# Optimization experiments

Hardware: AMD Instinct MI355X
Metric: run time of the kernel (lower is better)

The kernel has to match this reference:

```python
import jax, jax.numpy as jnp
import numpy as np

D_MODEL = 2048
N_HEADS = 16
D_HEAD = 128
BATCH = 2
SEQ = 2048
INIT_STD = 0.02
N_LAYERS = 12


def setup_inputs() -> dict:
    key = jax.random.key(0)
    ks = jax.random.split(key, 5)
    attn_std = INIT_STD
    proj_std = INIT_STD / np.sqrt(2 * N_LAYERS)
    return {
        "normalized_resid_pre": jax.random.normal(ks[0], (BATCH, SEQ, D_MODEL), jnp.float32),
        "W_Q": jax.random.normal(ks[1], (N_HEADS, D_MODEL, D_HEAD), jnp.float32) * attn_std,
        "W_K": jax.random.normal(ks[2], (N_HEADS, D_MODEL, D_HEAD), jnp.float32) * attn_std,
        "W_V": jax.random.normal(ks[3], (N_HEADS, D_MODEL, D_HEAD), jnp.float32) * attn_std,
        "W_O": jax.random.normal(ks[4], (N_HEADS, D_HEAD, D_MODEL), jnp.float32) * proj_std,
        "b_Q": jnp.zeros((N_HEADS, D_HEAD), jnp.float32),
        "b_K": jnp.zeros((N_HEADS, D_HEAD), jnp.float32),
        "b_V": jnp.zeros((N_HEADS, D_HEAD), jnp.float32),
        "b_O": jnp.zeros((D_MODEL,), jnp.float32),
    }


def reference(normalized_resid_pre, W_Q, W_K, W_V, W_O, b_Q, b_K, b_V, b_O):
    x = normalized_resid_pre
    # q,k,v: [batch, posn, nheads, d_head]
    q = jnp.einsum('bsd,hde->bshe', x, W_Q) + b_Q
    k = jnp.einsum('bsd,hde->bshe', x, W_K) + b_K
    v = jnp.einsum('bsd,hde->bshe', x, W_V) + b_V
    # scores: [batch, nheads, posn_Q, posn_K]
    scores = jnp.einsum('bqhe,bkhe->bhqk', q, k) / jnp.sqrt(jnp.float32(D_HEAD))
    S = scores.shape[-1]
    causal = jnp.tril(jnp.ones((S, S), bool))
    scores = jnp.where(causal, scores, jnp.float32(-jnp.inf))
    pattern = jax.nn.softmax(scores, axis=-1)
    z = jnp.einsum('bhqk,bkhe->bqhe', pattern, v)
    attn_out = jnp.einsum('bqhe,hed->bqd', z, W_O) + b_O
    return attn_out
```

## Files before the change

kernel.cpp:

```cpp
#include <hip/hip_runtime.h>
#include <hip/hip_bf16.h>

typedef __hip_bfloat16 bf16;
typedef __attribute__((ext_vector_type(8))) short bf16x8;
typedef __attribute__((ext_vector_type(4))) short bf16x4;
typedef __attribute__((ext_vector_type(4))) float f32x4;

#define D_MODEL 2048
#define SEQ     2048
#define NH      16
#define DH      128
#define BATCH   2
#define MTOT    (BATCH*SEQ)

__device__ __forceinline__ void async_cp16(const bf16* g, bf16* l) {
    __builtin_amdgcn_global_load_lds(
        (const __attribute__((address_space(1))) void*)g,
        (__attribute__((address_space(3))) void*)l, 16, 0, 0);
}

__device__ __forceinline__ short bf16bits(float f) {
    bf16 b = __float2bfloat16(f);
    return *reinterpret_cast<short*>(&b);
}

__global__ __launch_bounds__(256) void cvt_k(const float* __restrict__ in,
                                             bf16* __restrict__ out) {
    const long i = ((long)blockIdx.x * 256 + threadIdx.x) * 8;
    float4 a = *(const float4*)(in + i);
    float4 b = *(const float4*)(in + i + 4);
    __align__(16) bf16 t[8];
    t[0] = __float2bfloat16(a.x); t[1] = __float2bfloat16(a.y);
    t[2] = __float2bfloat16(a.z); t[3] = __float2bfloat16(a.w);
    t[4] = __float2bfloat16(b.x); t[5] = __float2bfloat16(b.y);
    t[6] = __float2bfloat16(b.z); t[7] = __float2bfloat16(b.w);
    *(bf16x8*)(out + i) = *(const bf16x8*)t;
}

__global__ __launch_bounds__(256) void transpose_cvt3_k(
    const float* __restrict__ in0, const float* __restrict__ in1,
    const float* __restrict__ in2,
    bf16* __restrict__ out, int R, int Cn, int mats_per_src)
{
    __shared__ float t[32][33];
    const int z = blockIdx.z;
    const int src = z / mats_per_src, mat = z % mats_per_src;
    const float* in = (src == 0) ? in0 : (src == 1) ? in1 : in2;
    const float* inm = in + (long)mat * R * Cn;
    bf16* outm = out + (long)z * R * Cn;
    const int c0 = blockIdx.x * 32, r0 = blockIdx.y * 32;
    const int tx = threadIdx.x & 31, ty = threadIdx.x >> 5;
#pragma unroll
    for (int i = 0; i < 4; ++i)
        t[ty + i*8][tx] = inm[(long)(r0 + ty + i*8) * Cn + c0 + tx];
    __syncthreads();
#pragma unroll
    for (int i = 0; i < 4; ++i)
        outm[(long)(c0 + ty + i*8) * R + r0 + tx] = __float2bfloat16(t[tx][ty + i*8]);
}

__global__ __launch_bounds__(256) void transpose_v_k(
    const bf16* __restrict__ V, bf16* __restrict__ VT)
{
    __shared__ bf16 t[32][33];
    const int bh = blockIdx.z;
    const int b = bh >> 4, h = bh & 15;
    const bf16* inm = V + (long)b*SEQ*D_MODEL + h*DH;
    bf16* outm = VT + (long)bh*DH*SEQ;
    const int r0 = blockIdx.x * 32;
    const int c0 = blockIdx.y * 32;
    const int tx = threadIdx.x & 31, ty = threadIdx.x >> 5;
#pragma unroll
    for (int i = 0; i < 4; ++i)
        t[ty + i*8][tx] = inm[(long)(r0 + ty + i*8)*D_MODEL + c0 + tx];
    __syncthreads();
#pragma unroll
    for (int i = 0; i < 4; ++i)
        outm[(long)(c0 + ty + i*8)*SEQ + r0 + tx] = t[tx][ty + i*8];
}

template <bool C_F32>
__device__ __forceinline__ void gemm128x128(
    const bf16* __restrict__ A, int lda,
    const bf16* __restrict__ Bt, int ldb,
    void* __restrict__ C, int ldc,
    const float* __restrict__ bias,
    int Kdim, int m0, int n0)
{
    __shared__ __align__(16) bf16 As[128*32];
    __shared__ __align__(16) bf16 Bs[128*32];
    const int tid  = threadIdx.x;
    const int wave = tid >> 6, lane = tid & 63;
    const int lr = lane & 15, lq = lane >> 4;
    const int wrow = wave >> 1, wcol = wave & 1;
    const int sr = lane >> 2, sk = (lane & 3) * 8;

    const f32x4 zero4 = {0.f, 0.f, 0.f, 0.f};
    f32x4 acc[4][4];
#pragma unroll
    for (int i = 0; i < 4; ++i)
#pragma unroll
        for (int j = 0; j < 4; ++j) acc[i][j] = zero4;

    for (int k0 = 0; k0 < Kdim; k0 += 32) {
#pragma unroll
        for (int c = 0; c < 2; ++c) {
            const int r = wave*32 + c*16;
            async_cp16(A  + (long)(m0 + r + sr)*lda + k0 + sk, As + r*32);
            async_cp16(Bt + (long)(n0 + r + sr)*ldb + k0 + sk, Bs + r*32);
        }
        __syncthreads();
        bf16x8 af[4], bfr[4];
#pragma unroll
        for (int i = 0; i < 4; ++i)
            af[i] = *(const bf16x8*)(As + (wrow*64 + i*16 + lr)*32 + lq*8);
#pragma unroll
        for (int j = 0; j < 4; ++j)
            bfr[j] = *(const bf16x8*)(Bs + (wcol*64 + j*16 + lr)*32 + lq*8);
#pragma unroll
        for (int i = 0; i < 4; ++i)
#pragma unroll
            for (int j = 0; j < 4; ++j)
                acc[i][j] = __builtin_amdgcn_mfma_f32_16x16x32_bf16(af[i], bfr[j], acc[i][j], 0, 0, 0);
        __syncthreads();
    }
#pragma unroll
    for (int j = 0; j < 4; ++j) {
        const int col = n0 + wcol*64 + j*16 + lr;
        const float bv = bias[col];
#pragma unroll
        for (int i = 0; i < 4; ++i) {
            const int row = m0 + wrow*64 + i*16 + lq*4;
#pragma unroll
            for (int r = 0; r < 4; ++r) {
                const float v = acc[i][j][r] + bv;
                if constexpr (C_F32) ((float*)C)[(long)(row + r)*ldc + col] = v;
                else ((bf16*)C)[(long)(row + r)*ldc + col] = __float2bfloat16(v);
            }
        }
    }
}

__global__ __launch_bounds__(256) void qkv_gemm_k(
    const bf16* __restrict__ X, const bf16* __restrict__ WT3,
    const float* __restrict__ bQ, const float* __restrict__ bK, const float* __restrict__ bV,
    bf16* __restrict__ Qo, bf16* __restrict__ Ko, bf16* __restrict__ Vo)
{
    const int mt  = blockIdx.x;
    const int sel = blockIdx.y >> 4;
    const int h   = blockIdx.y & 15;
    const float* bias; bf16* C;
    if (sel == 0)      { bias = bQ; C = Qo; }
    else if (sel == 1) { bias = bK; C = Ko; }
    else               { bias = bV; C = Vo; }
    gemm128x128<false>(X, D_MODEL, WT3 + (long)blockIdx.y*DH*D_MODEL, D_MODEL,
                       C + h*DH, NH*DH, bias + h*DH, D_MODEL, mt*128, 0);
}

__global__ __launch_bounds__(256) void out_gemm_k(
    const bf16* __restrict__ Z, const bf16* __restrict__ WOT,
    const float* __restrict__ bO, float* __restrict__ Out)
{
    gemm128x128<true>(Z, D_MODEL, WOT, D_MODEL, Out, D_MODEL, bO, D_MODEL,
                      (int)blockIdx.x*128, (int)blockIdx.y*128);
}

__global__ __launch_bounds__(512) void flash_k(
    const bf16* __restrict__ Q, const bf16* __restrict__ K,
    const bf16* __restrict__ VT, bf16* __restrict__ Z)
{
    __shared__ __align__(16) bf16 Ks[64*128];
    __shared__ __align__(16) bf16 Vts[128*64];
    __shared__ __align__(16) bf16 Ps[128*72];

    const int qt = (int)(gridDim.x - 1) - (int)blockIdx.x;
    const int bh = blockIdx.y;
    const int b  = bh >> 4, h = bh & 15;
    const long base = (long)b*SEQ*D_MODEL + h*DH;
    const bf16* Qb  = Q + base;
    const bf16* Kb  = K + base;
    const bf16* VTb = VT + (long)bh*DH*SEQ;
    bf16* Zb = Z + base;
    const int q0 = qt*128;
    const int tid = threadIdx.x, wave = tid >> 6, lane = tid & 63;
    const int lr = lane & 15, lq = lane >> 4;
    const int rx = lr & 7;

    const int ks_key_off = lane >> 4;
    const int ks_slot    = lane & 15;
    const int vt_row_off = lane >> 3;
    const int vt_slot    = lane & 7;

    bf16x8 aq[4];
#pragma unroll
    for (int ks = 0; ks < 4; ++ks)
        aq[ks] = *(const bf16x8*)(Qb + (long)(q0 + wave*16 + lr)*D_MODEL + ks*32 + lq*8);

    const f32x4 zero4 = {0.f, 0.f, 0.f, 0.f};
    f32x4 o_acc[8];
#pragma unroll
    for (int jf = 0; jf < 8; ++jf) o_acc[jf] = zero4;
    float m_run = -1e30f, l_run = 0.f;

    const float scale = 0.08838834764831845f;
    const int NT = 2*qt + 2;

    for (int kt = 0; kt < NT; ++kt) {
        const int k0 = kt*64;
        __syncthreads();
#pragma unroll
        for (int c2 = 0; c2 < 2; ++c2) {
            const int c = wave*2 + c2;
            const int key = c*4 + ks_key_off;
            async_cp16(Kb + (long)(k0 + key)*D_MODEL + ((ks_slot ^ (key & 7)) * 8),
                       Ks + c*512);
            const int f = c*8 + vt_row_off;
            async_cp16(VTb + (long)f*SEQ + k0 + ((vt_slot ^ (f & 7)) * 8),
                       Vts + c*512);
        }
        __syncthreads();

        const int rel_hi = q0 + wave*16 + 15 - k0;
        if (rel_hi >= 0) {
            f32x4 sc[4];
#pragma unroll
            for (int mt = 0; mt < 4; ++mt) sc[mt] = zero4;
            __builtin_amdgcn_s_setprio(1);
#pragma unroll
            for (int mt = 0; mt < 4; ++mt)
#pragma unroll
                for (int ks = 0; ks < 4; ++ks) {
                    bf16x8 bk = *(const bf16x8*)(Ks + (mt*16 + lr)*128 + (((ks*4 + lq) ^ rx) * 8));
                    sc[mt] = __builtin_amdgcn_mfma_f32_16x16x32_bf16(bk, aq[ks], sc[mt], 0, 0, 0);
                }
            __builtin_amdgcn_s_setprio(0);

            if (rel_hi < 78) {
                const int rel = q0 + wave*16 + lr - k0;
#pragma unroll
                for (int mt = 0; mt < 4; ++mt)
#pragma unroll
                    for (int r = 0; r < 4; ++r)
                        if (mt*16 + lq*4 + r > rel) sc[mt][r] = -1e30f;
            }

            float mx = sc[0][0];
#pragma unroll
            for (int mt = 0; mt < 4; ++mt)
#pragma unroll
                for (int r = 0; r < 4; ++r) mx = fmaxf(mx, sc[mt][r]);
            mx = fmaxf(mx, __shfl_xor(mx, 16, 64));
            mx = fmaxf(mx, __shfl_xor(mx, 32, 64));
            mx *= scale;

            if (!__all(mx - m_run <= 8.0f)) {
                const float mn = fmaxf(m_run, mx);
                const float al = __expf(m_run - mn);
                l_run *= al;
#pragma unroll
                for (int jf = 0; jf < 8; ++jf)
#pragma unroll
                    for (int r = 0; r < 4; ++r) o_acc[jf][r] *= al;
                m_run = mn;
            }

            float rs = 0.f;
#pragma unroll
            for (int mt = 0; mt < 4; ++mt)
#pragma unroll
                for (int r = 0; r < 4; ++r) {
                    const float p = __expf(fmaf(sc[mt][r], scale, -m_run));
                    sc[mt][r] = p;
                    rs += p;
                }
            rs += __shfl_xor(rs, 16, 64);
            rs += __shfl_xor(rs, 32, 64);
            l_run += rs;

#pragma unroll
            for (int mt = 0; mt < 4; ++mt) {
                bf16x4 pk;
#pragma unroll
                for (int r = 0; r < 4; ++r) pk[r] = bf16bits(sc[mt][r]);
                *(bf16x4*)(Ps + (wave*16 + lr)*72 + mt*16 + lq*4) = pk;
            }

            bf16x8 pb0 = *(const bf16x8*)(Ps + (wave*16 + lr)*72 + lq*8);
            bf16x8 pb1 = *(const bf16x8*)(Ps + (wave*16 + lr)*72 + 32 + lq*8);

            __builtin_amdgcn_s_setprio(1);
#pragma unroll
            for (int jf = 0; jf < 8; ++jf) {
                const int f = jf*16 + lr;
                bf16x8 av0 = *(const bf16x8*)(Vts + f*64 + ((lq ^ rx) * 8));
                bf16x8 av1 = *(const bf16x8*)(Vts + f*64 + (((4 + lq) ^ rx) * 8));
                o_acc[jf] = __builtin_amdgcn_mfma_f32_16x16x32_bf16(av0, pb0, o_acc[jf], 0, 0, 0);
                o_acc[jf] = __builtin_amdgcn_mfma_f32_16x16x32_bf16(av1, pb1, o_acc[jf], 0, 0, 0);
            }
            __builtin_amdgcn_s_setprio(0);
        }
    }

    const float inv = 1.f / l_run;
    const long zrow = (long)(q0 + wave*16 + lr) * D_MODEL;
#pragma unroll
    for (int jf = 0; jf < 8; ++jf) {
        bf16x4 pk;
#pragma unroll
        for (int r = 0; r < 4; ++r) pk[r] = bf16bits(o_acc[jf][r] * inv);
        *(bf16x4*)(Zb + zrow + jf*16 + lq*4) = pk;
    }
}

extern "C" void kernel_launch(void* const* d_in, const int* in_sizes, int n_in,
                              void* d_out, int out_size, void* d_ws, size_t ws_size,
                              hipStream_t stream) {
    const float* X  = (const float*)d_in[0];
    const float* WQ = (const float*)d_in[1];
    const float* WK = (const float*)d_in[2];
    const float* WV = (const float*)d_in[3];
    const float* WO = (const float*)d_in[4];
    const float* bQ = (const float*)d_in[5];
    const float* bK = (const float*)d_in[6];
    const float* bV = (const float*)d_in[7];
    const float* bO = (const float*)d_in[8];
    float* out = (float*)d_out;

    bf16* ws = (bf16*)d_ws;
    const long WSZ = (long)NH*DH*D_MODEL;
    const long MSZ = (long)MTOT*D_MODEL;
    bf16* Xb  = ws;
    bf16* WT3 = Xb + MSZ;
    bf16* WOT = WT3 + 3*WSZ;
    bf16* Qb  = WOT + WSZ;
    bf16* Kb  = Qb + MSZ;
    bf16* Vb  = Kb + MSZ;
    bf16* Zb  = Xb;
    bf16* VT  = WT3;

    cvt_k<<<MSZ/(256*8), 256, 0, stream>>>(X, Xb);
    transpose_cvt3_k<<<dim3(DH/32, D_MODEL/32, 3*NH), 256, 0, stream>>>(
        WQ, WK, WV, WT3, D_MODEL, DH, NH);
    transpose_cvt3_k<<<dim3(D_MODEL/32, D_MODEL/32, 1), 256, 0, stream>>>(
        WO, WO, WO, WOT, D_MODEL, D_MODEL, 1);

    qkv_gemm_k<<<dim3(MTOT/128, 48), 256, 0, stream>>>(Xb, WT3, bQ, bK, bV, Qb, Kb, Vb);
    transpose_v_k<<<dim3(SEQ/32, DH/32, BATCH*NH), 256, 0, stream>>>(Vb, VT);
    flash_k<<<dim3(SEQ/128, BATCH*NH), 512, 0, stream>>>(Qb, Kb, VT, Zb);
    out_gemm_k<<<dim3(MTOT/128, D_MODEL/128), 256, 0, stream>>>(Zb, WOT, bO, out);
}
```

Before: 407.9 us.

## Replace QKV projection with 256x256-tile, 8-wave pipelined GEMM kernel

Swaps the 128x128 QKV GEMM for a new 256x256 tile kernel with 512 threads. It uses double-buffered async global-to-LDS loads with XOR swizzling, interleaves staging of the next K-slice with MFMA phases, and raises wave priority around the MFMA blocks. The larger tile raises arithmetic intensity and cuts redundant global reads of X and weights. In exchange it uses 128KB of LDS and 128 accumulator registers per thread, which limits occupancy, and the grid shrinks to 16x24 blocks.

```diff
diff --git a/kernel.cpp b/kernel.cpp
--- a/kernel.cpp
+++ b/kernel.cpp
@@ -23,6 +23,9 @@
     bf16 b = __float2bfloat16(f);
     return *reinterpret_cast<short*>(&b);
 }
+
+#define GBAR() do { asm volatile("" ::: "memory"); __builtin_amdgcn_s_barrier(); \
+                    asm volatile("" ::: "memory"); } while (0)
 
 __global__ __launch_bounds__(256) void cvt_k(const float* __restrict__ in,
                                              bf16* __restrict__ out) {
@@ -141,28 +144,157 @@
     }
 }
 
-__global__ __launch_bounds__(256) void qkv_gemm_k(
-    const bf16* __restrict__ X, const bf16* __restrict__ WT3,
-    const float* __restrict__ bQ, const float* __restrict__ bK, const float* __restrict__ bV,
-    bf16* __restrict__ Qo, bf16* __restrict__ Ko, bf16* __restrict__ Vo)
-{
-    const int mt  = blockIdx.x;
-    const int sel = blockIdx.y >> 4;
-    const int h   = blockIdx.y & 15;
-    const float* bias; bf16* C;
-    if (sel == 0)      { bias = bQ; C = Qo; }
-    else if (sel == 1) { bias = bK; C = Ko; }
-    else               { bias = bV; C = Vo; }
-    gemm128x128<false>(X, D_MODEL, WT3 + (long)blockIdx.y*DH*D_MODEL, D_MODEL,
-                       C + h*DH, NH*DH, bias + h*DH, D_MODEL, mt*128, 0);
-}
-
 __global__ __launch_bounds__(256) void out_gemm_k(
     const bf16* __restrict__ Z, const bf16* __restrict__ WOT,
     const float* __restrict__ bO, float* __restrict__ Out)
 {
     gemm128x128<true>(Z, D_MODEL, WOT, D_MODEL, Out, D_MODEL, bO, D_MODEL,
                       (int)blockIdx.x*128, (int)blockIdx.y*128);
+}
+
+__global__ __launch_bounds__(512, 2) void qkv_gemm256_k(
+    const bf16* __restrict__ A, const bf16* __restrict__ Bt,
+    const float* __restrict__ bQ, const float* __restrict__ bK, const float* __restrict__ bV,
+    bf16* __restrict__ Qo, bf16* __restrict__ Ko, bf16* __restrict__ Vo)
+{
+    __shared__ __align__(16) bf16 lds[65536];
+    bf16* As = lds;
+    bf16* Bs = lds + 32768;
+
+    const int m0 = blockIdx.x * 256;
+    const int n0 = blockIdx.y * 256;
+    const int tid = threadIdx.x, wave = tid >> 6, lane = tid & 63;
+    const int wm = wave >> 2, wn = wave & 3;
+    const int lr = lane & 15, lq = lane >> 4;
+    const int sph = (lr >> 1) & 3;
+
+    const int s_r  = lane >> 2;
+    const int s_sl = lane & 3;
+
+    auto stageA = [&](int t, int kh) {
+        const int k = t*64 + kh*32;
+        bf16* u = As + (((t & 1)*2 + kh) << 13);
+#pragma unroll
+        for (int i = 0; i < 2; ++i) {
+            const int c = wave*2 + i;
+            const int r = c*16 + s_r;
+            async_cp16(A + (long)(m0 + r)*D_MODEL + k + ((s_sl ^ ((r >> 1) & 3)) * 8),
+                       u + c*512);
+        }
+    };
+    auto stageB = [&](int t, int kh) {
+        const int k = t*64 + kh*32;
+        bf16* u = Bs + (((t & 1)*2 + kh) << 13);
+#pragma unroll
+        for (int i = 0; i < 2; ++i) {
+            const int c = wave*2 + i;
+            const int r = c*16 + s_r;
+            async_cp16(Bt + (long)(n0 + r)*D_MODEL + k + ((s_sl ^ ((r >> 1) & 3)) * 8),
+                       u + c*512);
+        }
+    };
+    auto rdA = [&](int t, int kh, int fm) -> bf16x8 {
+        const int r = wm*128 + fm*16 + lr;
+        return *(const bf16x8*)(As + (((t & 1)*2 + kh) << 13) + r*32 + ((lq ^ sph) * 8));
+    };
+    auto rdB = [&](int t, int kh, int fn) -> bf16x8 {
+        const int r = wn*64 + fn*16 + lr;
+        return *(const bf16x8*)(Bs + (((t & 1)*2 + kh) << 13) + r*32 + ((lq ^ sph) * 8));
+    };
+
+    const f32x4 zero4 = {0.f, 0.f, 0.f, 0.f};
+    f32x4 acc[8][4];
+#pragma unroll
+    for (int i = 0; i < 8; ++i)
+#pragma unroll
+        for (int j = 0; j < 4; ++j) acc[i][j] = zero4;
+
+    const int NT = D_MODEL / 64;
+
+    stageA(0, 0); stageB(0, 0);
+    stageA(0, 1); stageB(0, 1);
+    stageA(1, 0); stageB(1, 0);
+    asm volatile("s_waitcnt vmcnt(4)" ::: "memory");
+    GBAR();
+
+    for (int t = 0; t < NT; ++t) {
+        bf16x8 aF[4], bF[4];
+
+#pragma unroll
+        for (int j = 0; j < 4; ++j) aF[j] = rdA(t, 0, j);
+#pragma unroll
+        for (int j = 0; j < 4; ++j) bF[j] = rdB(t, 0, j);
+        if (t + 1 < NT) stageA(t + 1, 1);
+        GBAR();
+        __builtin_amdgcn_s_setprio(1);
+#pragma unroll
+        for (int j = 0; j < 4; ++j)
+#pragma unroll
+            for (int fn = 0; fn < 4; ++fn)
+                acc[j][fn] = __builtin_amdgcn_mfma_f32_16x16x32_bf16(aF[j], bF[fn], acc[j][fn], 0, 0, 0);
+        __builtin_amdgcn_s_setprio(0);
+        GBAR();
+
+#pragma unroll
+        for (int j = 0; j < 4; ++j) aF[j] = rdA(t, 0, 4 + j);
+        if (t + 1 < NT) stageB(t + 1, 1);
+        GBAR();
+        __builtin_amdgcn_s_setprio(1);
+#pragma unroll
+        for (int j = 0; j < 4; ++j)
+#pragma unroll
+            for (int fn = 0; fn < 4; ++fn)
+                acc[4 + j][fn] = __builtin_amdgcn_mfma_f32_16x16x32_bf16(aF[j], bF[fn], acc[4 + j][fn], 0, 0, 0);
+        __builtin_amdgcn_s_setprio(0);
+        GBAR();
+
+#pragma unroll
+        for (int j = 0; j < 4; ++j) aF[j] = rdA(t, 1, j);
+#pragma unroll
+        for (int j = 0; j < 4; ++j) bF[j] = rdB(t, 1, j);
+        if (t + 2 < NT) stageA(t + 2, 0);
+        GBAR();
+        __builtin_amdgcn_s_setprio(1);
+#pragma unroll
+        for (int j = 0; j < 4; ++j)
+#pragma unroll
+            for (int fn = 0; fn < 4; ++fn)
+                acc[j][fn] = __builtin_amdgcn_mfma_f32_16x16x32_bf16(aF[j], bF[fn], acc[j][fn], 0, 0, 0);
+        __builtin_amdgcn_s_setprio(0);
+        GBAR();
+
+#pragma unroll
+        for (int j = 0; j < 4; ++j) aF[j] = rdA(t, 1, 4 + j);
+        if (t + 2 < NT) stageB(t + 2, 0);
+        GBAR();
+        __builtin_amdgcn_s_setprio(1);
+#pragma unroll
+        for (int j = 0; j < 4; ++j)
+#pragma unroll
+            for (int fn = 0; fn < 4; ++fn)
+                acc[4 + j][fn] = __builtin_amdgcn_mfma_f32_16x16x32_bf16(aF[j], bF[fn], acc[4 + j][fn], 0, 0, 0);
+        __builtin_amdgcn_s_setprio(0);
+        if (t < NT - 2) asm volatile("s_waitcnt vmcnt(4)" ::: "memory");
+        else            asm volatile("s_waitcnt vmcnt(0)" ::: "memory");
+        GBAR();
+    }
+
+    const int gc0 = n0 + wn*64;
+    const int sel = gc0 >> 11;
+    bf16* C        = (sel == 0) ? Qo : (sel == 1) ? Ko : Vo;
+    const float* bs = (sel == 0) ? bQ : (sel == 1) ? bK : bV;
+#pragma unroll
+    for (int fn = 0; fn < 4; ++fn) {
+        const int dcol = (gc0 + fn*16 + lr) & 2047;
+        const float bv = bs[dcol];
+#pragma unroll
+        for (int fm = 0; fm < 8; ++fm) {
+            const int row = m0 + wm*128 + fm*16 + lq*4;
+#pragma unroll
+            for (int rr = 0; rr < 4; ++rr)
+                C[(long)(row + rr)*D_MODEL + dcol] = __float2bfloat16(acc[fm][fn][rr] + bv);
+        }
+    }
 }
 
 __global__ __launch_bounds__(512) void flash_k(
@@ -344,7 +476,8 @@
     transpose_cvt3_k<<<dim3(D_MODEL/32, D_MODEL/32, 1), 256, 0, stream>>>(
         WO, WO, WO, WOT, D_MODEL, D_MODEL, 1);
 
-    qkv_gemm_k<<<dim3(MTOT/128, 48), 256, 0, stream>>>(Xb, WT3, bQ, bK, bV, Qb, Kb, Vb);
+    qkv_gemm256_k<<<dim3(MTOT/256, 3*D_MODEL/256), 512, 0, stream>>>(
+        Xb, WT3, bQ, bK, bV, Qb, Kb, Vb);
     transpose_v_k<<<dim3(SEQ/32, DH/32, BATCH*NH), 256, 0, stream>>>(Vb, VT);
     flash_k<<<dim3(SEQ/128, BATCH*NH), 512, 0, stream>>>(Qb, Kb, VT, Zb);
     out_gemm_k<<<dim3(MTOT/128, D_MODEL/128), 256, 0, stream>>>(Zb, WOT, bO, out);
```

Result: no change. 410.6 us (+0.7%).

## Replace QKV GEMM with 128x256 tile, 8-wave, triple-buffered async-LDS kernel

Applied to the files above, without the earlier changes.

Replaces the 128x128-tile QKV projection kernel with a new kernel using 128x256 tiles, 512 threads, and a three-slot async global-to-LDS pipeline with an XOR-swizzled layout. A 1D grid is remapped so that blocks on the same XCD share N columns, which aims to improve L2 reuse. Fewer redundant A-tile loads and deeper prefetch are meant to raise MFMA utilization. In exchange the kernel needs more LDS and registers per block, which can lower occupancy.

```diff
diff --git a/kernel.cpp b/kernel.cpp
--- a/kernel.cpp
+++ b/kernel.cpp
@@ -23,6 +23,9 @@
     bf16 b = __float2bfloat16(f);
     return *reinterpret_cast<short*>(&b);
 }
+
+#define GBAR() do { asm volatile("" ::: "memory"); __builtin_amdgcn_s_barrier(); \
+                    asm volatile("" ::: "memory"); } while (0)
 
 __global__ __launch_bounds__(256) void cvt_k(const float* __restrict__ in,
                                              bf16* __restrict__ out) {
@@ -141,28 +144,116 @@
     }
 }
 
-__global__ __launch_bounds__(256) void qkv_gemm_k(
-    const bf16* __restrict__ X, const bf16* __restrict__ WT3,
-    const float* __restrict__ bQ, const float* __restrict__ bK, const float* __restrict__ bV,
-    bf16* __restrict__ Qo, bf16* __restrict__ Ko, bf16* __restrict__ Vo)
-{
-    const int mt  = blockIdx.x;
-    const int sel = blockIdx.y >> 4;
-    const int h   = blockIdx.y & 15;
-    const float* bias; bf16* C;
-    if (sel == 0)      { bias = bQ; C = Qo; }
-    else if (sel == 1) { bias = bK; C = Ko; }
-    else               { bias = bV; C = Vo; }
-    gemm128x128<false>(X, D_MODEL, WT3 + (long)blockIdx.y*DH*D_MODEL, D_MODEL,
-                       C + h*DH, NH*DH, bias + h*DH, D_MODEL, mt*128, 0);
-}
-
 __global__ __launch_bounds__(256) void out_gemm_k(
     const bf16* __restrict__ Z, const bf16* __restrict__ WOT,
     const float* __restrict__ bO, float* __restrict__ Out)
 {
     gemm128x128<true>(Z, D_MODEL, WOT, D_MODEL, Out, D_MODEL, bO, D_MODEL,
                       (int)blockIdx.x*128, (int)blockIdx.y*128);
+}
+
+__global__ __launch_bounds__(512) void qkv_gemm_k2(
+    const bf16* __restrict__ A, const bf16* __restrict__ Bt,
+    const float* __restrict__ bQ, const float* __restrict__ bK, const float* __restrict__ bV,
+    bf16* __restrict__ Qo, bf16* __restrict__ Ko, bf16* __restrict__ Vo)
+{
+    __shared__ __align__(16) bf16 lds[36864];
+    bf16* As = lds;
+    bf16* Bs = lds + 12288;
+
+    const int lin = blockIdx.x;
+    const int xcd = lin & 7, idx = lin >> 3;
+    const int m0 = (idx & 31) * 128;
+    const int n0 = (xcd * 3 + (idx >> 5)) * 256;
+
+    const int tid = threadIdx.x, wave = tid >> 6, lane = tid & 63;
+    const int wm = wave >> 2, wn = wave & 3;
+    const int lr = lane & 15, lq = lane >> 4;
+    const int sph = (lr >> 1) & 3;
+
+    const int s_r  = lane >> 2;
+    const int s_sl = lane & 3;
+
+    auto stageA = [&](int t, int slot) {
+        const int k = t * 32;
+        const int r = wave*16 + s_r;
+        async_cp16(A + (long)(m0 + r)*D_MODEL + k + ((s_sl ^ ((r >> 1) & 3)) * 8),
+                   As + slot*4096 + wave*512);
+    };
+    auto stageB = [&](int t, int slot) {
+        const int k = t * 32;
+#pragma unroll
+        for (int i = 0; i < 2; ++i) {
+            const int c = wave*2 + i;
+            const int r = c*16 + s_r;
+            async_cp16(Bt + (long)(n0 + r)*D_MODEL + k + ((s_sl ^ ((r >> 1) & 3)) * 8),
+                       Bs + slot*8192 + c*512);
+        }
+    };
+    auto rdA = [&](int slot, int fm) -> bf16x8 {
+        const int r = wm*64 + fm*16 + lr;
+        return *(const bf16x8*)(As + slot*4096 + r*32 + ((lq ^ sph) * 8));
+    };
+    auto rdB = [&](int slot, int fn) -> bf16x8 {
+        const int r = wn*64 + fn*16 + lr;
+        return *(const bf16x8*)(Bs + slot*8192 + r*32 + ((lq ^ sph) * 8));
+    };
+
+    const f32x4 zero4 = {0.f, 0.f, 0.f, 0.f};
+    f32x4 acc[4][4];
+#pragma unroll
+    for (int i = 0; i < 4; ++i)
+#pragma unroll
+        for (int j = 0; j < 4; ++j) acc[i][j] = zero4;
+
+    const int NT = D_MODEL / 32;
+
+    stageA(0, 0); stageB(0, 0);
+    stageA(1, 1); stageB(1, 1);
+    asm volatile("s_waitcnt vmcnt(3)" ::: "memory");
+    GBAR();
+
+    int cur = 0, s2 = 2;
+    for (int t = 0; t < NT; ++t) {
+        bf16x8 aF[4], bF[4];
+#pragma unroll
+        for (int j = 0; j < 4; ++j) aF[j] = rdA(cur, j);
+#pragma unroll
+        for (int j = 0; j < 4; ++j) bF[j] = rdB(cur, j);
+        if (t + 2 < NT) { stageA(t + 2, s2); stageB(t + 2, s2); }
+
+        __builtin_amdgcn_s_setprio(1);
+#pragma unroll
+        for (int fm = 0; fm < 4; ++fm)
+#pragma unroll
+            for (int fn = 0; fn < 4; ++fn)
+                acc[fm][fn] = __builtin_amdgcn_mfma_f32_16x16x32_bf16(aF[fm], bF[fn], acc[fm][fn], 0, 0, 0);
+        __builtin_amdgcn_s_setprio(0);
+
+        if (t + 2 < NT) asm volatile("s_waitcnt vmcnt(3)" ::: "memory");
+        else            asm volatile("s_waitcnt vmcnt(0)" ::: "memory");
+        GBAR();
+
+        cur = (cur == 2) ? 0 : cur + 1;
+        s2  = (s2  == 2) ? 0 : s2  + 1;
+    }
+
+    const int gc0 = n0 + wn*64;
+    const int sel = gc0 >> 11;
+    bf16* C        = (sel == 0) ? Qo : (sel == 1) ? Ko : Vo;
+    const float* bs = (sel == 0) ? bQ : (sel == 1) ? bK : bV;
+#pragma unroll
+    for (int fn = 0; fn < 4; ++fn) {
+        const int dcol = (gc0 + fn*16 + lr) & 2047;
+        const float bv = bs[dcol];
+#pragma unroll
+        for (int fm = 0; fm < 4; ++fm) {
+            const int row = m0 + wm*64 + fm*16 + lq*4;
+#pragma unroll
+            for (int rr = 0; rr < 4; ++rr)
+                C[(long)(row + rr)*D_MODEL + dcol] = __float2bfloat16(acc[fm][fn][rr] + bv);
+        }
+    }
 }
 
 __global__ __launch_bounds__(512) void flash_k(
@@ -344,7 +435,8 @@
     transpose_cvt3_k<<<dim3(D_MODEL/32, D_MODEL/32, 1), 256, 0, stream>>>(
         WO, WO, WO, WOT, D_MODEL, D_MODEL, 1);
 
-    qkv_gemm_k<<<dim3(MTOT/128, 48), 256, 0, stream>>>(Xb, WT3, bQ, bK, bV, Qb, Kb, Vb);
+    qkv_gemm_k2<<<dim3((MTOT/128)*(3*D_MODEL/256)), 512, 0, stream>>>(
+        Xb, WT3, bQ, bK, bV, Qb, Kb, Vb);
     transpose_v_k<<<dim3(SEQ/32, DH/32, BATCH*NH), 256, 0, stream>>>(Vb, VT);
     flash_k<<<dim3(SEQ/128, BATCH*NH), 512, 0, stream>>>(Qb, Kb, VT, Zb);
     out_gemm_k<<<dim3(MTOT/128, D_MODEL/128), 256, 0, stream>>>(Zb, WOT, bO, out);
```

Measured after the change: 408.0 us. About the same (+0.0%).
